# Optimization experiments

Measured on AMD Instinct MI355X. Metric: run time of the kernel, lower is better.

The kernel has to match this reference:

```python
import jax, jax.numpy as jnp
import numpy as np

B, S, D, H = 4, 2048, 1024, 4
HD = D // H


def setup_inputs() -> dict:
    key = jax.random.key(0)
    ks = jax.random.split(key, 6)
    s = 0.02  # init scale for projection weights
    return {
        "hidden_states": jax.random.normal(ks[0], (B, S, D), jnp.float32),
        "Wq": jax.random.normal(ks[1], (D, D), jnp.float32) * s,
        "Wk": jax.random.normal(ks[2], (D, D), jnp.float32) * s,
        "Wv": jax.random.normal(ks[3], (D, D), jnp.float32) * s,
        "Wo": jax.random.normal(ks[4], (D, D), jnp.float32) * s,
        "bo": jnp.zeros((D,), jnp.float32),
        "betas": jax.random.normal(ks[5], (1, H, 1, 1), jnp.float32),
        "mem": jnp.zeros((H, HD, HD), jnp.float32),
        "z": jnp.zeros((H, HD, 1), jnp.float32),
    }


def reference(hidden_states, Wq, Wk, Wv, Wo, bo, betas, mem, z):
    b, s, d = hidden_states.shape
    h = betas.shape[1]
    hd = d // h

    def split(x):  # [b,s,d] -> [b,h,s,hd]
        return x.reshape(b, s, h, hd).transpose(0, 2, 1, 3)

    q = split(hidden_states @ Wq.T)
    k = split(hidden_states @ Wk.T)
    v = split(hidden_states @ Wv.T)

    # standard causal attention (note: no 1/sqrt(d) scaling, faithful to source)
    aw = jnp.einsum('bhqd,bhkd->bhqk', q, k)
    causal = jnp.tril(jnp.ones((s, s), bool))
    aw = jnp.where(causal, aw, jnp.finfo(aw.dtype).min)
    p = jax.nn.softmax(aw, axis=-1)
    attn = jnp.einsum('bhqk,bhkd->bhqd', p, v)

    # linear-attention memory read
    sq = jax.nn.elu(q) + 1.0
    sk = jax.nn.elu(k) + 1.0
    A_mem = jnp.einsum('bhsd,hde->bhse', sq, mem) / (
        jnp.einsum('bhsd,hdo->bhso', sq, z) + 1e-6)

    # sigmoid-gated blend
    g = jax.nn.sigmoid(betas)
    out = g * A_mem + (1.0 - g) * attn

    # memory / z state update (delta rule), averaged over batch
    delta = jnp.einsum('bhsd,hde->bhse', sk, mem) / (
        jnp.einsum('bhsd,hdo->bhso', sk, z) + 1e-6)
    mem_new = mem + jnp.einsum('bhsd,bhse->hde', sk, v - delta) / b
    z_new = z + jnp.mean(jnp.sum(sk, axis=2), axis=0)[:, :, None]

    # merge heads + output projection
    out = out.transpose(0, 2, 1, 3).reshape(b, s, d)
    out = out @ Wo.T + bo
    return (out, mem_new, z_new)
```

## Files before the change

kernel.cpp:

```cpp
#include <hip/hip_runtime.h>

#define Bsz 4
#define Ssz 2048
#define Dsz 1024
#define Hsz 4
#define HDsz 256
#define Msz 8192

typedef unsigned short u16;
typedef __attribute__((ext_vector_type(8))) short bf16x8;
typedef __attribute__((ext_vector_type(4))) float f32x4;

__device__ __forceinline__ u16 f2b(float f) {
  unsigned u = __float_as_uint(f);
  return (u16)((u + 0x7FFFu + ((u >> 16) & 1u)) >> 16);
}
__device__ __forceinline__ unsigned pk2(float a, float b) {
  return (unsigned)f2b(a) | ((unsigned)f2b(b) << 16);
}

typedef const unsigned int __attribute__((address_space(1)))* gcp;
typedef unsigned int __attribute__((address_space(3)))* lcp;
__device__ __forceinline__ void gld16(const u16* g, u16* l) {
  __builtin_amdgcn_global_load_lds((gcp)g, (lcp)l, 16, 0, 0);
}

__global__ __launch_bounds__(256) void cvt_bf16(const float4* __restrict__ in,
                                                u16* __restrict__ outp) {
  size_t i = (size_t)blockIdx.x * 256 + threadIdx.x;
  float4 v = in[i];
  uint2 r; r.x = pk2(v.x, v.y); r.y = pk2(v.z, v.w);
  *(uint2*)(outp + i * 4) = r;
}

__global__ __launch_bounds__(256) void gemm_lds(const u16* __restrict__ A16,
                                                const u16* __restrict__ Wb,
                                                const float* __restrict__ bias,
                                                float* __restrict__ C32,
                                                u16* __restrict__ Cbf) {
  __shared__ u16 sA[128 * 32];
  __shared__ u16 sB[128 * 32];
  const int tid = threadIdx.x;
  const int lane = tid & 63, quad = lane >> 4, l15 = lane & 15;
  const int w = tid >> 6;
  const int mw = (w >> 1) * 64, nw = (w & 1) * 64;
  const int bid = blockIdx.y * 8 + blockIdx.x;
  const int nb = (bid & 7) * 64 + (bid >> 3);
  const int m0 = (nb >> 3) * 128, n0 = (nb & 7) * 128;
  const int r0 = tid >> 2, seg = (tid & 3) * 8;
  const u16* ga0 = A16 + (size_t)(m0 + r0) * Dsz + seg;
  const u16* gb0 = Wb + (size_t)(n0 + r0) * Dsz + seg;
  u16* lA0 = sA + w * 512;
  u16* lA1 = sA + 2048 + w * 512;
  u16* lB0 = sB + w * 512;
  u16* lB1 = sB + 2048 + w * 512;
  f32x4 acc[4][4] = {};
  for (int k0 = 0; k0 < Dsz; k0 += 32) {
    __syncthreads();
    gld16(ga0 + k0, lA0);
    gld16(ga0 + (size_t)64 * Dsz + k0, lA1);
    gld16(gb0 + k0, lB0);
    gld16(gb0 + (size_t)64 * Dsz + k0, lB1);
    __syncthreads();
    bf16x8 af[4], bfr[4];
#pragma unroll
    for (int i = 0; i < 4; ++i) {
      af[i] = *(const bf16x8*)&sA[(mw + i * 16 + l15) * 32 + quad * 8];
      bfr[i] = *(const bf16x8*)&sB[(nw + i * 16 + l15) * 32 + quad * 8];
    }
#pragma unroll
    for (int i = 0; i < 4; ++i)
#pragma unroll
      for (int j = 0; j < 4; ++j)
        acc[i][j] = __builtin_amdgcn_mfma_f32_16x16x32_bf16(af[i], bfr[j], acc[i][j], 0, 0, 0);
  }
#pragma unroll
  for (int j = 0; j < 4; ++j) {
    const int n = n0 + nw + j * 16 + l15;
    const float bv = bias ? bias[n] : 0.f;
#pragma unroll
    for (int i = 0; i < 4; ++i) {
#pragma unroll
      for (int r = 0; r < 4; ++r) {
        const int m = m0 + mw + i * 16 + quad * 4 + r;
        const float val = acc[i][j][r] + bv;
        const size_t idx = (size_t)m * Dsz + n;
        if (C32) C32[idx] = val;
        if (Cbf) Cbf[idx] = f2b(val);
      }
    }
  }
}

__global__ __launch_bounds__(256) void transpose_v(const float* __restrict__ V,
                                                   u16* __restrict__ Vt) {
  __shared__ u16 tile[32 * 36];
  const int t = threadIdx.x;
  const int s0 = blockIdx.x * 32, e0 = blockIdx.y * 32, bh = blockIdx.z;
  const int b = bh >> 2, h = bh & 3;
  {
    const int s_l = t >> 3, e8 = (t & 7) * 4;
    float4 v = *(const float4*)(V + ((size_t)(b * Ssz) + s0 + s_l) * Dsz + h * HDsz + e0 + e8);
    uint2 r; r.x = pk2(v.x, v.y); r.y = pk2(v.z, v.w);
    *(uint2*)&tile[s_l * 36 + e8] = r;
  }
  __syncthreads();
  {
    const int e_l = t >> 3, s4 = (t & 7) * 4;
    u16 a = tile[(s4 + 0) * 36 + e_l], b2 = tile[(s4 + 1) * 36 + e_l];
    u16 c = tile[(s4 + 2) * 36 + e_l], d = tile[(s4 + 3) * 36 + e_l];
    uint2 r; r.x = (unsigned)a | ((unsigned)b2 << 16);
    r.y = (unsigned)c | ((unsigned)d << 16);
    *(uint2*)(Vt + ((size_t)bh * HDsz + e0 + e_l) * Ssz + s0 + s4) = r;
  }
}

__global__ __launch_bounds__(256) void attn_mfma(const u16* __restrict__ Qg,
                                                 const u16* __restrict__ Kg,
                                                 const u16* __restrict__ Vtg,
                                                 float* __restrict__ At,
                                                 float* __restrict__ Pb,
                                                 float* __restrict__ mlb) {
  static const unsigned char tab[52] = {
      (unsigned char)(31|0x80), (unsigned char)(31|0xC0),
      (unsigned char)(30|0x80), (unsigned char)(30|0xC0),
      (unsigned char)(29|0x80), (unsigned char)(29|0xC0),
      (unsigned char)(28|0x80), (unsigned char)(28|0xC0),
      (unsigned char)(27|0x80), (unsigned char)(27|0xC0),
      (unsigned char)(26|0x80), (unsigned char)(26|0xC0),
      (unsigned char)(25|0x80), (unsigned char)(25|0xC0),
      (unsigned char)(24|0x80), (unsigned char)(24|0xC0),
      (unsigned char)(23|0x80), (unsigned char)(23|0xC0),
      11,
      (unsigned char)(22|0x80), (unsigned char)(22|0xC0),
      (unsigned char)(21|0x80), (unsigned char)(21|0xC0),
      10,
      (unsigned char)(20|0x80), (unsigned char)(20|0xC0),
      (unsigned char)(19|0x80), (unsigned char)(19|0xC0),
      9,
      (unsigned char)(18|0x80), (unsigned char)(18|0xC0),
      (unsigned char)(17|0x80), (unsigned char)(17|0xC0),
      8,
      (unsigned char)(16|0x80), (unsigned char)(16|0xC0),
      (unsigned char)(15|0x80), (unsigned char)(15|0xC0),
      7,
      (unsigned char)(14|0x80), (unsigned char)(14|0xC0),
      (unsigned char)(13|0x80), (unsigned char)(13|0xC0),
      6,
      (unsigned char)(12|0x80), (unsigned char)(12|0xC0),
      5, 4, 3, 2, 1, 0};
  const int e = tab[blockIdx.x];
  const int qt = e & 63, cc = (e >> 6) & 1;
  const bool split = (e >> 7) != 0;
  const int bh = blockIdx.y, b = bh >> 2, h = bh & 3;
  const int tid = threadIdx.x, w = tid >> 6, lane = tid & 63;
  const int quad = lane >> 4, l15 = lane & 15;
  __shared__ u16 sK[2][32 * 256];
  __shared__ u16 sV[256 * 32];
  const int q0w = qt * 64 + w * 16;
  bf16x8 qf[8];
  {
    const u16* qp = Qg + ((size_t)(b * Ssz) + q0w + l15) * Dsz + h * HDsz + quad * 8;
#pragma unroll
    for (int dd = 0; dd < 8; ++dd) qf[dd] = *(const bf16x8*)(qp + dd * 32);
  }
  f32x4 o[16] = {};
  float m_old = -1e30f, l = 0.f;
  const int nkt = 2 * qt + 2, half = qt + 1;
  const int kt_lo = (split && cc) ? half : 0;
  const int kt_hi = (split && !cc) ? half : nkt;
  const u16* kstage = Kg + ((size_t)(b * Ssz) + (tid >> 5)) * Dsz + h * HDsz
                      + (((tid & 31) ^ ((tid >> 5) & 7)) << 3);
  const u16* vstage = Vtg + ((size_t)bh * HDsz + (tid >> 2)) * Ssz
                      + (((tid & 3) ^ ((tid >> 3) & 3)) << 3);
  int bufc = 0;
  {
    const u16* kp = kstage + (size_t)(kt_lo * 32) * Dsz;
#pragma unroll
    for (int i = 0; i < 4; ++i)
      gld16(kp + (size_t)i * 8 * Dsz, &sK[0][w * 512 + i * 2048]);
  }
  for (int kt = kt_lo; kt < kt_hi; ++kt) {
    const int j0 = kt * 32;
    __syncthreads();
    {
      const u16* vp = vstage + kt * 32;
#pragma unroll
      for (int i = 0; i < 4; ++i)
        gld16(vp + (size_t)i * 64 * Ssz, &sV[w * 512 + i * 2048]);
    }
    if (kt + 1 < kt_hi) {
      const u16* kp = kstage + (size_t)((kt + 1) * 32) * Dsz;
      const int bn = bufc ^ 1;
#pragma unroll
      for (int i = 0; i < 4; ++i)
        gld16(kp + (size_t)i * 8 * Dsz, &sK[bn][w * 512 + i * 2048]);
    }
    f32x4 s0a = {}, s0b = {}, s1a = {}, s1b = {};
#pragma unroll
    for (int dd = 0; dd < 4; ++dd) {
      const int c0 = ((dd * 4 + quad) ^ (l15 & 7)) << 3;
      const int c1 = (((dd + 4) * 4 + quad) ^ (l15 & 7)) << 3;
      bf16x8 a0 = *(const bf16x8*)&sK[bufc][l15 * 256 + c0];
      bf16x8 a1 = *(const bf16x8*)&sK[bufc][(16 + l15) * 256 + c0];
      bf16x8 b0 = *(const bf16x8*)&sK[bufc][l15 * 256 + c1];
      bf16x8 b1 = *(const bf16x8*)&sK[bufc][(16 + l15) * 256 + c1];
      s0a = __builtin_amdgcn_mfma_f32_16x16x32_bf16(a0, qf[dd], s0a, 0, 0, 0);
      s1a = __builtin_amdgcn_mfma_f32_16x16x32_bf16(a1, qf[dd], s1a, 0, 0, 0);
      s0b = __builtin_amdgcn_mfma_f32_16x16x32_bf16(b0, qf[dd + 4], s0b, 0, 0, 0);
      s1b = __builtin_amdgcn_mfma_f32_16x16x32_bf16(b1, qf[dd + 4], s1b, 0, 0, 0);
    }
    f32x4 s0v = s0a + s0b, s1v = s1a + s1b;
    const int qg = q0w + l15;
    float p[8];
#pragma unroll
    for (int r = 0; r < 4; ++r) {
      const int kg = j0 + quad * 4 + r;
      p[r] = (kg <= qg) ? s0v[r] : -1e30f;
      p[4 + r] = (kg + 16 <= qg) ? s1v[r] : -1e30f;
    }
    float mt = p[0];
#pragma unroll
    for (int i = 1; i < 8; ++i) mt = fmaxf(mt, p[i]);
    mt = fmaxf(mt, __shfl_xor(mt, 16));
    mt = fmaxf(mt, __shfl_xor(mt, 32));
    const float m_new = fmaxf(m_old, mt);
    const float alpha = __expf(m_old - m_new);
    float ts = 0.f;
#pragma unroll
    for (int i = 0; i < 8; ++i) { p[i] = __expf(p[i] - m_new); ts += p[i]; }
    ts += __shfl_xor(ts, 16);
    ts += __shfl_xor(ts, 32);
    l = l * alpha + ts;
    m_old = m_new;
    if (!__all(alpha == 1.0f)) {
      const float a0_ = __shfl(alpha, (lane & 48) | (quad * 4 + 0));
      const float a1_ = __shfl(alpha, (lane & 48) | (quad * 4 + 1));
      const float a2_ = __shfl(alpha, (lane & 48) | (quad * 4 + 2));
      const float a3_ = __shfl(alpha, (lane & 48) | (quad * 4 + 3));
#pragma unroll
      for (int ds = 0; ds < 16; ++ds) {
        o[ds][0] *= a0_; o[ds][1] *= a1_; o[ds][2] *= a2_; o[ds][3] *= a3_;
      }
    }
    float xx[8];
#pragma unroll
    for (int i = 0; i < 8; ++i) xx[i] = __shfl_xor(p[i], 16);
    const bool qe = (quad & 1) == 0;
    float Alo[8], Ahi[8];
#pragma unroll
    for (int i = 0; i < 4; ++i) {
      Alo[i] = qe ? p[i] : xx[i];
      Alo[4 + i] = qe ? xx[i] : p[i];
      Ahi[i] = qe ? p[4 + i] : xx[4 + i];
      Ahi[4 + i] = qe ? xx[4 + i] : p[4 + i];
    }
    float zz[8];
    const bool sendlo = (quad & 1) != 0;
#pragma unroll
    for (int i = 0; i < 8; ++i) zz[i] = __shfl_xor(sendlo ? Alo[i] : Ahi[i], 32);
    float fin[8];
#pragma unroll
    for (int i = 0; i < 8; ++i)
      fin[i] = (quad == 0) ? Alo[i] : (quad == 3) ? Ahi[i] : zz[i];
    uint4 pkv;
    pkv.x = pk2(fin[0], fin[1]); pkv.y = pk2(fin[2], fin[3]);
    pkv.z = pk2(fin[4], fin[5]); pkv.w = pk2(fin[6], fin[7]);
    bf16x8 pf = *(bf16x8*)&pkv;
    const int vc0 = (quad ^ ((l15 >> 1) & 3)) << 3;
    __syncthreads();
#pragma unroll
    for (int ds = 0; ds < 16; ++ds) {
      bf16x8 bv = *(const bf16x8*)&sV[(ds * 16 + l15) * 32 + vc0];
      o[ds] = __builtin_amdgcn_mfma_f32_16x16x32_bf16(pf, bv, o[ds], 0, 0, 0);
    }
    bufc ^= 1;
  }
  if (!split) {
    float lr[4];
#pragma unroll
    for (int r = 0; r < 4; ++r) lr[r] = 1.f / __shfl(l, (lane & 48) | (quad * 4 + r));
    float* ob = At + ((size_t)bh * Ssz + q0w + quad * 4) * HDsz + l15;
#pragma unroll
    for (int r = 0; r < 4; ++r)
#pragma unroll
      for (int ds = 0; ds < 16; ++ds)
        ob[(size_t)r * HDsz + ds * 16] = o[ds][r] * lr[r];
  } else {
    float* dst;
    if (cc == 0)
      dst = At + ((size_t)bh * Ssz + q0w + quad * 4) * HDsz + l15;
    else
      dst = Pb + ((size_t)((bh * 20 + (qt - 12)) * 64) + w * 16 + quad * 4) * HDsz + l15;
#pragma unroll
    for (int r = 0; r < 4; ++r)
#pragma unroll
      for (int ds = 0; ds < 16; ++ds)
        dst[(size_t)r * HDsz + ds * 16] = o[ds][r];
    if (lane < 16) {
      const int idx = (bh * 20 + (qt - 12)) * 64 + w * 16 + l15;
      mlb[cc * 40960 + idx] = m_old;
      mlb[cc * 40960 + 20480 + idx] = l;
    }
  }
}

__global__ __launch_bounds__(256) void attn_merge(float* __restrict__ At,
                                                  const float* __restrict__ Pb,
                                                  const float* __restrict__ mlb) {
  const int qx = blockIdx.x, bh = blockIdx.y;
  const int t = threadIdx.x;
  const int slot = (bh * 20 + qx) * 64;
  float4* abase = (float4*)(At + ((size_t)bh * Ssz + (12 + qx) * 64) * HDsz);
  const float4* pbase = (const float4*)(Pb + (size_t)slot * HDsz);
#pragma unroll
  for (int i = 0; i < 16; ++i) {
    const int f = i * 256 + t;
    const int qr = f >> 6;
    const int idx = slot + qr;
    const float m0 = mlb[idx], l0 = mlb[20480 + idx];
    const float m1 = mlb[40960 + idx], l1 = mlb[61440 + idx];
    const float mm = fmaxf(m0, m1);
    const float w0 = __expf(m0 - mm), w1 = __expf(m1 - mm);
    const float inv = 1.f / (l0 * w0 + l1 * w1);
    float4 av = abase[f];
    float4 pv = pbase[f];
    float4 ov;
    ov.x = (av.x * w0 + pv.x * w1) * inv;
    ov.y = (av.y * w0 + pv.y * w1) * inv;
    ov.z = (av.z * w0 + pv.z * w1) * inv;
    ov.w = (av.w * w0 + pv.w * w1) * inv;
    abase[f] = ov;
  }
}

__global__ __launch_bounds__(256) void eludens(float* __restrict__ Qb,
                                               float* __restrict__ Kb,
                                               const float* __restrict__ z,
                                               float* __restrict__ dq,
                                               float* __restrict__ dk) {
  const int wid = threadIdx.x >> 6, lane = threadIdx.x & 63;
  const int r = blockIdx.x * 4 + wid;
  const int b = r >> 13, h = (r >> 11) & 3, s = r & 2047;
  const size_t base = ((size_t)(b * Ssz + s)) * Dsz + h * HDsz + lane * 4;
  float4 z4 = *(const float4*)(z + h * HDsz + lane * 4);
  float4 q = *(float4*)(Qb + base);
  q.x = q.x > 0.f ? q.x + 1.f : __expf(q.x);
  q.y = q.y > 0.f ? q.y + 1.f : __expf(q.y);
  q.z = q.z > 0.f ? q.z + 1.f : __expf(q.z);
  q.w = q.w > 0.f ? q.w + 1.f : __expf(q.w);
  *(float4*)(Qb + base) = q;
  float4 k = *(float4*)(Kb + base);
  k.x = k.x > 0.f ? k.x + 1.f : __expf(k.x);
  k.y = k.y > 0.f ? k.y + 1.f : __expf(k.y);
  k.z = k.z > 0.f ? k.z + 1.f : __expf(k.z);
  k.w = k.w > 0.f ? k.w + 1.f : __expf(k.w);
  *(float4*)(Kb + base) = k;
  float pq = q.x * z4.x + q.y * z4.y + q.z * z4.z + q.w * z4.w;
  float pk = k.x * z4.x + k.y * z4.y + k.z * z4.z + k.w * z4.w;
#pragma unroll
  for (int off = 32; off; off >>= 1) {
    pq += __shfl_down(pq, off);
    pk += __shfl_down(pk, off);
  }
  if (lane == 0) { dq[r] = pq; dk[r] = pk; }
}

__global__ __launch_bounds__(256) void memread_mfma(const float* __restrict__ Asrc,
                                                    const float* __restrict__ mem,
                                                    const float* __restrict__ dens,
                                                    const float* __restrict__ betas,
                                                    const float* __restrict__ At,
                                                    float* __restrict__ Vio,
                                                    u16* __restrict__ bfout, int mode) {
  const int h = blockIdx.z;
  const int tid = threadIdx.x, lane = tid & 63, w = tid >> 6;
  const int quad = lane >> 4, l15 = lane & 15;
  const int mw = (w >> 1) * 64, ew = (w & 1) * 64;
  const int m0 = blockIdx.y * 128, e0t = blockIdx.x * 128;
  __shared__ u16 sA[128 * 40];
  __shared__ u16 sB[128 * 40];
  const int srow = tid >> 1, sseg = (tid & 1) * 16;
  const int k4 = (tid & 7) * 4, e4 = (tid >> 3) * 4;
  f32x4 acc[4][4] = {};
  for (int k0 = 0; k0 < HDsz; k0 += 32) {
    __syncthreads();
    {
      const float* ap = Asrc + (size_t)(m0 + srow) * Dsz + h * HDsz + k0 + sseg;
      float4 f0 = *(const float4*)ap, f1 = *(const float4*)(ap + 4);
      float4 f2 = *(const float4*)(ap + 8), f3 = *(const float4*)(ap + 12);
      uint4 u0, u1;
      u0.x = pk2(f0.x, f0.y); u0.y = pk2(f0.z, f0.w);
      u0.z = pk2(f1.x, f1.y); u0.w = pk2(f1.z, f1.w);
      u1.x = pk2(f2.x, f2.y); u1.y = pk2(f2.z, f2.w);
      u1.z = pk2(f3.x, f3.y); u1.w = pk2(f3.z, f3.w);
      u16* dst = &sA[srow * 40 + sseg];
      *(uint4*)dst = u0; *(uint4*)(dst + 8) = u1;
    }
    {
      const float* bp = mem + (size_t)h * 65536 + (size_t)(k0 + k4) * HDsz + e0t + e4;
      float4 r0 = *(const float4*)bp;
      float4 r1 = *(const float4*)(bp + HDsz);
      float4 r2 = *(const float4*)(bp + 2 * HDsz);
      float4 r3 = *(const float4*)(bp + 3 * HDsz);
      const float* rr[4] = {(const float*)&r0, (const float*)&r1,
                            (const float*)&r2, (const float*)&r3};
#pragma unroll
      for (int c = 0; c < 4; ++c) {
        uint2 u;
        u.x = pk2(rr[0][c], rr[1][c]);
        u.y = pk2(rr[2][c], rr[3][c]);
        *(uint2*)&sB[(e4 + c) * 40 + k4] = u;
      }
    }
    __syncthreads();
    bf16x8 af[4], bfr[4];
#pragma unroll
    for (int i = 0; i < 4; ++i) {
      af[i] = *(const bf16x8*)&sA[(mw + i * 16 + l15) * 40 + quad * 8];
      bfr[i] = *(const bf16x8*)&sB[(ew + i * 16 + l15) * 40 + quad * 8];
    }
#pragma unroll
    for (int i = 0; i < 4; ++i)
#pragma unroll
      for (int j = 0; j < 4; ++j)
        acc[i][j] = __builtin_amdgcn_mfma_f32_16x16x32_bf16(af[i], bfr[j], acc[i][j], 0, 0, 0);
  }
  const float g = 1.f / (1.f + __expf(-betas[h]));
#pragma unroll
  for (int i = 0; i < 4; ++i) {
#pragma unroll
    for (int r = 0; r < 4; ++r) {
      const int m = m0 + mw + i * 16 + quad * 4 + r;
      const int b = m >> 11, s = m & 2047;
      const int rowidx = ((b << 2) + h) * Ssz + s;
      const float inv = 1.f / (dens[rowidx] + 1e-6f);
#pragma unroll
      for (int j = 0; j < 4; ++j) {
        const int e = e0t + ew + j * 16 + l15;
        const float av = acc[i][j][r] * inv;
        if (mode == 0) {
          const float a = At[(size_t)rowidx * HDsz + e];
          bfout[(size_t)m * Dsz + h * HDsz + e] = f2b(g * av + (1.f - g) * a);
        } else {
          float* p = Vio + (size_t)m * Dsz + h * HDsz + e;
          *p = *p - av;
        }
      }
    }
  }
}

__global__ __launch_bounds__(256) void mem_update_mfma(const float* __restrict__ SK,
                                                       const float* __restrict__ W,
                                                       float* __restrict__ P) {
  const int de = blockIdx.x;
  const int d0 = (de >> 1) * 128, e0 = (de & 1) * 128;
  const int h = blockIdx.y, chunk = blockIdx.z;
  const int m0 = chunk * 512;
  const int tid = threadIdx.x, lane = tid & 63, w = tid >> 6;
  const int quad = lane >> 4, l15 = lane & 15;
  const int dw = (w >> 1) * 64, ew = (w & 1) * 64;
  __shared__ u16 sA[128 * 40];
  __shared__ u16 sB[128 * 40];
  const int m4 = (tid & 7) * 4;
  const int c4 = (tid >> 3) * 4;
  f32x4 acc[4][4] = {};
  for (int mt = 0; mt < 512; mt += 32) {
    __syncthreads();
    const float* ka = SK + (size_t)(m0 + mt + m4) * Dsz + h * HDsz + d0 + c4;
    const float* wa = W + (size_t)(m0 + mt + m4) * Dsz + h * HDsz + e0 + c4;
    float4 a0 = *(const float4*)ka;
    float4 a1 = *(const float4*)(ka + Dsz);
    float4 a2 = *(const float4*)(ka + 2 * Dsz);
    float4 a3 = *(const float4*)(ka + 3 * Dsz);
    float4 b0 = *(const float4*)wa;
    float4 b1 = *(const float4*)(wa + Dsz);
    float4 b2 = *(const float4*)(wa + 2 * Dsz);
    float4 b3 = *(const float4*)(wa + 3 * Dsz);
    const float* aa[4] = {(const float*)&a0, (const float*)&a1,
                          (const float*)&a2, (const float*)&a3};
    const float* bb[4] = {(const float*)&b0, (const float*)&b1,
                          (const float*)&b2, (const float*)&b3};
#pragma unroll
    for (int c = 0; c < 4; ++c) {
      uint2 ua, ub2;
      ua.x = pk2(aa[0][c], aa[1][c]); ua.y = pk2(aa[2][c], aa[3][c]);
      ub2.x = pk2(bb[0][c], bb[1][c]); ub2.y = pk2(bb[2][c], bb[3][c]);
      *(uint2*)&sA[(c4 + c) * 40 + m4] = ua;
      *(uint2*)&sB[(c4 + c) * 40 + m4] = ub2;
    }
    __syncthreads();
    bf16x8 af[4], bfr[4];
#pragma unroll
    for (int i = 0; i < 4; ++i) {
      af[i] = *(const bf16x8*)&sA[(dw + i * 16 + l15) * 40 + quad * 8];
      bfr[i] = *(const bf16x8*)&sB[(ew + i * 16 + l15) * 40 + quad * 8];
    }
#pragma unroll
    for (int i = 0; i < 4; ++i)
#pragma unroll
      for (int j = 0; j < 4; ++j)
        acc[i][j] = __builtin_amdgcn_mfma_f32_16x16x32_bf16(af[i], bfr[j], acc[i][j], 0, 0, 0);
  }
  float* Pp = P + ((size_t)(h * 16 + chunk)) * 65536;
#pragma unroll
  for (int i = 0; i < 4; ++i)
#pragma unroll
    for (int r = 0; r < 4; ++r) {
      const int d = d0 + dw + i * 16 + quad * 4 + r;
#pragma unroll
      for (int j = 0; j < 4; ++j) {
        const int e = e0 + ew + j * 16 + l15;
        Pp[(size_t)d * HDsz + e] = acc[i][j][r];
      }
    }
}

__global__ __launch_bounds__(256) void mem_reduce(const float4* __restrict__ P,
                                                  const float4* __restrict__ mem,
                                                  float4* __restrict__ outmem) {
  const int gid = blockIdx.x * 256 + threadIdx.x;
  const int h = gid >> 14, off = gid & 16383;
  float sx = 0.f, sy = 0.f, sz = 0.f, sw = 0.f;
#pragma unroll 4
  for (int c = 0; c < 16; ++c) {
    float4 v = P[((size_t)(h * 16 + c) << 14) + off];
    sx += v.x; sy += v.y; sz += v.z; sw += v.w;
  }
  float4 m = mem[gid];
  float4 o;
  o.x = m.x + 0.25f * sx; o.y = m.y + 0.25f * sy;
  o.z = m.z + 0.25f * sz; o.w = m.w + 0.25f * sw;
  outmem[gid] = o;
}

__global__ __launch_bounds__(256) void z_update(const float* __restrict__ SK,
                                                const float* __restrict__ z_in,
                                                float* __restrict__ z_out) {
  __shared__ float4 red[256];
  const int h = blockIdx.x >> 7, chunk = blockIdx.x & 127;
  const int wid = threadIdx.x >> 6, lane = threadIdx.x & 63;
  const int m0 = chunk * 64;
  float4 s = {0.f, 0.f, 0.f, 0.f};
#pragma unroll
  for (int i = 0; i < 16; ++i) {
    const int row = m0 + i * 4 + wid;
    float4 v = *(const float4*)(SK + (size_t)row * Dsz + h * HDsz + lane * 4);
    s.x += v.x; s.y += v.y; s.z += v.z; s.w += v.w;
  }
  red[wid * 64 + lane] = s;
  __syncthreads();
  if (wid == 0) {
    float4 a = red[lane], b = red[64 + lane], c = red[128 + lane], d = red[192 + lane];
    a.x = (a.x + b.x + c.x + d.x) * 0.25f;
    a.y = (a.y + b.y + c.y + d.y) * 0.25f;
    a.z = (a.z + b.z + c.z + d.z) * 0.25f;
    a.w = (a.w + b.w + c.w + d.w) * 0.25f;
    if (chunk == 0) {
      const float4 z4 = *(const float4*)(z_in + h * HDsz + lane * 4);
      a.x += z4.x; a.y += z4.y; a.z += z4.z; a.w += z4.w;
    }
    float* zp = z_out + h * HDsz + lane * 4;
    atomicAdd(zp + 0, a.x);
    atomicAdd(zp + 1, a.y);
    atomicAdd(zp + 2, a.z);
    atomicAdd(zp + 3, a.w);
  }
}

extern "C" void kernel_launch(void* const* d_in, const int* in_sizes, int n_in,
                              void* d_out, int out_size, void* d_ws, size_t ws_size,
                              hipStream_t stream) {
  (void)in_sizes; (void)n_in; (void)out_size; (void)ws_size;
  const float* Hs = (const float*)d_in[0];
  const float* Wq = (const float*)d_in[1];
  const float* Wk = (const float*)d_in[2];
  const float* Wv = (const float*)d_in[3];
  const float* Wo = (const float*)d_in[4];
  const float* bo = (const float*)d_in[5];
  const float* betas = (const float*)d_in[6];
  const float* mem = (const float*)d_in[7];
  const float* z = (const float*)d_in[8];

  float* ws = (float*)d_ws;
  float* Qb = ws;
  float* Kb = ws + 8388608;
  float* Vb = ws + 16777216;
  float* At = ws + 25165824;
  float* dq = ws + 33554432;
  float* dk = ws + 33587200;
  float* mlb = ws + 33619968;
  u16* ub = (u16*)(ws + 33701888);
  u16* Wqb = ub;
  u16* Wkb = ub + 1048576;
  u16* Wvb = ub + 2097152;
  u16* Wob = ub + 3145728;
  u16* Qbf = ub + 4194304;
  u16* Kbf = ub + 12582912;
  u16* Vt = ub + 20971520;
  u16* Hsb = Vt;
  float* P = (float*)Vt;
  float* Pb = (float*)d_out;

  float* out = (float*)d_out;
  float* outmem = out + (size_t)Msz * Dsz;
  float* outz = outmem + Hsz * HDsz * HDsz;

  hipMemsetAsync(outz, 0, (size_t)(Hsz * HDsz) * sizeof(float), stream);

  cvt_bf16<<<1024, 256, 0, stream>>>((const float4*)Wq, Wqb);
  cvt_bf16<<<1024, 256, 0, stream>>>((const float4*)Wk, Wkb);
  cvt_bf16<<<1024, 256, 0, stream>>>((const float4*)Wv, Wvb);
  cvt_bf16<<<1024, 256, 0, stream>>>((const float4*)Wo, Wob);
  cvt_bf16<<<8192, 256, 0, stream>>>((const float4*)Hs, Hsb);

  dim3 gg(8, 64);
  gemm_lds<<<gg, 256, 0, stream>>>(Hsb, Wqb, nullptr, Qb, Qbf);
  gemm_lds<<<gg, 256, 0, stream>>>(Hsb, Wkb, nullptr, Kb, Kbf);
  gemm_lds<<<gg, 256, 0, stream>>>(Hsb, Wvb, nullptr, Vb, nullptr);

  transpose_v<<<dim3(64, 8, 16), 256, 0, stream>>>(Vb, Vt);
  attn_mfma<<<dim3(52, 16), 256, 0, stream>>>(Qbf, Kbf, Vt, At, Pb, mlb);
  attn_merge<<<dim3(20, 16), 256, 0, stream>>>(At, Pb, mlb);

  eludens<<<8192, 256, 0, stream>>>(Qb, Kb, z, dq, dk);

  memread_mfma<<<dim3(2, 64, 4), 256, 0, stream>>>(Qb, mem, dq, betas, At, nullptr, Qbf, 0);
  memread_mfma<<<dim3(2, 64, 4), 256, 0, stream>>>(Kb, mem, dk, betas, nullptr, Vb, nullptr, 1);

  mem_update_mfma<<<dim3(4, 4, 16), 256, 0, stream>>>(Kb, Vb, P);
  mem_reduce<<<256, 256, 0, stream>>>((const float4*)P, (const float4*)mem, (float4*)outmem);
  z_update<<<512, 256, 0, stream>>>(Kb, z, outz);

  gemm_lds<<<gg, 256, 0, stream>>>(Qbf, Wob, bo, out, nullptr);
}
```

Before: 523.7 us.

## Deepen GEMM K-tile with swizzled LDS and streamline attention softmax

The GEMM now stages a 64-wide K slice per iteration with an XOR-swizzled LDS layout. This halves the number of barrier pairs and aims to avoid bank conflicts on fragment reads. The attention softmax switches to base-2 exponentials by folding log2(e) into the bf16 Q copy. It also skips rescaling of the running max unless the max grows by more than a threshold, and packs P to bf16 before a cheaper shuffle-based layout exchange. The lazy-rescale threshold risks larger intermediate values, and the merge kernel now uses exp2 on maxima that live in the log2 domain.

```diff
diff --git a/kernel.cpp b/kernel.cpp
--- a/kernel.cpp
+++ b/kernel.cpp
@@ -6,6 +6,7 @@
 #define Hsz 4
 #define HDsz 256
 #define Msz 8192
+#define LOG2E 1.4426950408889634f
 
 typedef unsigned short u16;
 typedef __attribute__((ext_vector_type(8))) short bf16x8;
@@ -17,6 +18,13 @@
 }
 __device__ __forceinline__ unsigned pk2(float a, float b) {
   return (unsigned)f2b(a) | ((unsigned)f2b(b) << 16);
+}
+__device__ __forceinline__ float ex2(float x) {
+#if __has_builtin(__builtin_amdgcn_exp2f)
+  return __builtin_amdgcn_exp2f(x);
+#else
+  return exp2f(x);
+#endif
 }
 
 typedef const unsigned int __attribute__((address_space(1)))* gcp;
@@ -37,9 +45,10 @@
                                                 const u16* __restrict__ Wb,
                                                 const float* __restrict__ bias,
                                                 float* __restrict__ C32,
-                                                u16* __restrict__ Cbf) {
-  __shared__ u16 sA[128 * 32];
-  __shared__ u16 sB[128 * 32];
+                                                u16* __restrict__ Cbf,
+                                                float cbfs) {
+  __shared__ u16 sA[128 * 64];
+  __shared__ u16 sB[128 * 64];
   const int tid = threadIdx.x;
   const int lane = tid & 63, quad = lane >> 4, l15 = lane & 15;
   const int w = tid >> 6;
@@ -47,32 +56,34 @@
   const int bid = blockIdx.y * 8 + blockIdx.x;
   const int nb = (bid & 7) * 64 + (bid >> 3);
   const int m0 = (nb >> 3) * 128, n0 = (nb & 7) * 128;
-  const int r0 = tid >> 2, seg = (tid & 3) * 8;
+  const int r0 = tid >> 3;
+  const int seg = ((tid & 7) ^ (r0 & 7)) * 8;
   const u16* ga0 = A16 + (size_t)(m0 + r0) * Dsz + seg;
   const u16* gb0 = Wb + (size_t)(n0 + r0) * Dsz + seg;
-  u16* lA0 = sA + w * 512;
-  u16* lA1 = sA + 2048 + w * 512;
-  u16* lB0 = sB + w * 512;
-  u16* lB1 = sB + 2048 + w * 512;
   f32x4 acc[4][4] = {};
-  for (int k0 = 0; k0 < Dsz; k0 += 32) {
-    __syncthreads();
-    gld16(ga0 + k0, lA0);
-    gld16(ga0 + (size_t)64 * Dsz + k0, lA1);
-    gld16(gb0 + k0, lB0);
-    gld16(gb0 + (size_t)64 * Dsz + k0, lB1);
-    __syncthreads();
-    bf16x8 af[4], bfr[4];
+  for (int k0 = 0; k0 < Dsz; k0 += 64) {
+    __syncthreads();
 #pragma unroll
     for (int i = 0; i < 4; ++i) {
-      af[i] = *(const bf16x8*)&sA[(mw + i * 16 + l15) * 32 + quad * 8];
-      bfr[i] = *(const bf16x8*)&sB[(nw + i * 16 + l15) * 32 + quad * 8];
-    }
-#pragma unroll
-    for (int i = 0; i < 4; ++i)
-#pragma unroll
-      for (int j = 0; j < 4; ++j)
-        acc[i][j] = __builtin_amdgcn_mfma_f32_16x16x32_bf16(af[i], bfr[j], acc[i][j], 0, 0, 0);
+      gld16(ga0 + (size_t)(i * 32) * Dsz + k0, sA + i * 2048 + w * 512);
+      gld16(gb0 + (size_t)(i * 32) * Dsz + k0, sB + i * 2048 + w * 512);
+    }
+    __syncthreads();
+#pragma unroll
+    for (int dd = 0; dd < 2; ++dd) {
+      bf16x8 af[4], bfr[4];
+#pragma unroll
+      for (int i = 0; i < 4; ++i) {
+        const int sl = ((quad + 4 * dd) ^ (l15 & 7)) * 8;
+        af[i] = *(const bf16x8*)&sA[(mw + i * 16 + l15) * 64 + sl];
+        bfr[i] = *(const bf16x8*)&sB[(nw + i * 16 + l15) * 64 + sl];
+      }
+#pragma unroll
+      for (int i = 0; i < 4; ++i)
+#pragma unroll
+        for (int j = 0; j < 4; ++j)
+          acc[i][j] = __builtin_amdgcn_mfma_f32_16x16x32_bf16(af[i], bfr[j], acc[i][j], 0, 0, 0);
+    }
   }
 #pragma unroll
   for (int j = 0; j < 4; ++j) {
@@ -86,7 +97,7 @@
         const float val = acc[i][j][r] + bv;
         const size_t idx = (size_t)m * Dsz + n;
         if (C32) C32[idx] = val;
-        if (Cbf) Cbf[idx] = f2b(val);
+        if (Cbf) Cbf[idx] = f2b(val * cbfs);
       }
     }
   }
@@ -219,21 +230,23 @@
       p[r] = (kg <= qg) ? s0v[r] : -1e30f;
       p[4 + r] = (kg + 16 <= qg) ? s1v[r] : -1e30f;
     }
-    float mt = p[0];
-#pragma unroll
-    for (int i = 1; i < 8; ++i) mt = fmaxf(mt, p[i]);
+    float mt = fmaxf(fmaxf(fmaxf(p[0], p[1]), fmaxf(p[2], p[3])),
+                     fmaxf(fmaxf(p[4], p[5]), fmaxf(p[6], p[7])));
     mt = fmaxf(mt, __shfl_xor(mt, 16));
     mt = fmaxf(mt, __shfl_xor(mt, 32));
-    const float m_new = fmaxf(m_old, mt);
-    const float alpha = __expf(m_old - m_new);
+    const bool keep = __all(mt - m_old <= 11.0f);
+    const float m_new = keep ? m_old : fmaxf(m_old, mt);
     float ts = 0.f;
 #pragma unroll
-    for (int i = 0; i < 8; ++i) { p[i] = __expf(p[i] - m_new); ts += p[i]; }
+    for (int i = 0; i < 8; ++i) { p[i] = ex2(p[i] - m_new); ts += p[i]; }
     ts += __shfl_xor(ts, 16);
     ts += __shfl_xor(ts, 32);
-    l = l * alpha + ts;
-    m_old = m_new;
-    if (!__all(alpha == 1.0f)) {
+    if (keep) {
+      l += ts;
+    } else {
+      const float alpha = ex2(m_old - m_new);
+      l = l * alpha + ts;
+      m_old = m_new;
       const float a0_ = __shfl(alpha, (lane & 48) | (quad * 4 + 0));
       const float a1_ = __shfl(alpha, (lane & 48) | (quad * 4 + 1));
       const float a2_ = __shfl(alpha, (lane & 48) | (quad * 4 + 2));
@@ -243,29 +256,20 @@
         o[ds][0] *= a0_; o[ds][1] *= a1_; o[ds][2] *= a2_; o[ds][3] *= a3_;
       }
     }
-    float xx[8];
-#pragma unroll
-    for (int i = 0; i < 8; ++i) xx[i] = __shfl_xor(p[i], 16);
-    const bool qe = (quad & 1) == 0;
-    float Alo[8], Ahi[8];
-#pragma unroll
-    for (int i = 0; i < 4; ++i) {
-      Alo[i] = qe ? p[i] : xx[i];
-      Alo[4 + i] = qe ? xx[i] : p[i];
-      Ahi[i] = qe ? p[4 + i] : xx[4 + i];
-      Ahi[4 + i] = qe ? xx[4 + i] : p[4 + i];
-    }
-    float zz[8];
-    const bool sendlo = (quad & 1) != 0;
-#pragma unroll
-    for (int i = 0; i < 8; ++i) zz[i] = __shfl_xor(sendlo ? Alo[i] : Ahi[i], 32);
-    float fin[8];
-#pragma unroll
-    for (int i = 0; i < 8; ++i)
-      fin[i] = (quad == 0) ? Alo[i] : (quad == 3) ? Ahi[i] : zz[i];
+    const unsigned a0p = pk2(p[0], p[1]), a1p = pk2(p[2], p[3]);
+    const unsigned b0p = pk2(p[4], p[5]), b1p = pk2(p[6], p[7]);
+    const int sAl = l15 | ((quad & 1) << 5);
+    const int sBl = sAl | 16;
+    const unsigned xa0 = __shfl(a0p, sAl), xa1 = __shfl(a1p, sAl);
+    const unsigned xb0 = __shfl(b0p, sAl), xb1 = __shfl(b1p, sAl);
+    const unsigned ya0 = __shfl(a0p, sBl), ya1 = __shfl(a1p, sBl);
+    const unsigned yb0 = __shfl(b0p, sBl), yb1 = __shfl(b1p, sBl);
+    const bool hi2 = quad >= 2;
     uint4 pkv;
-    pkv.x = pk2(fin[0], fin[1]); pkv.y = pk2(fin[2], fin[3]);
-    pkv.z = pk2(fin[4], fin[5]); pkv.w = pk2(fin[6], fin[7]);
+    pkv.x = hi2 ? xb0 : xa0;
+    pkv.y = hi2 ? xb1 : xa1;
+    pkv.z = hi2 ? yb0 : ya0;
+    pkv.w = hi2 ? yb1 : ya1;
     bf16x8 pf = *(bf16x8*)&pkv;
     const int vc0 = (quad ^ ((l15 >> 1) & 3)) << 3;
     __syncthreads();
@@ -321,7 +325,7 @@
     const float m0 = mlb[idx], l0 = mlb[20480 + idx];
     const float m1 = mlb[40960 + idx], l1 = mlb[61440 + idx];
     const float mm = fmaxf(m0, m1);
-    const float w0 = __expf(m0 - mm), w1 = __expf(m1 - mm);
+    const float w0 = ex2(m0 - mm), w1 = ex2(m1 - mm);
     const float inv = 1.f / (l0 * w0 + l1 * w1);
     float4 av = abase[f];
     float4 pv = pbase[f];
@@ -616,9 +620,9 @@
   cvt_bf16<<<8192, 256, 0, stream>>>((const float4*)Hs, Hsb);
 
   dim3 gg(8, 64);
-  gemm_lds<<<gg, 256, 0, stream>>>(Hsb, Wqb, nullptr, Qb, Qbf);
-  gemm_lds<<<gg, 256, 0, stream>>>(Hsb, Wkb, nullptr, Kb, Kbf);
-  gemm_lds<<<gg, 256, 0, stream>>>(Hsb, Wvb, nullptr, Vb, nullptr);
+  gemm_lds<<<gg, 256, 0, stream>>>(Hsb, Wqb, nullptr, Qb, Qbf, LOG2E);
+  gemm_lds<<<gg, 256, 0, stream>>>(Hsb, Wkb, nullptr, Kb, Kbf, 1.f);
+  gemm_lds<<<gg, 256, 0, stream>>>(Hsb, Wvb, nullptr, Vb, nullptr, 1.f);
 
   transpose_v<<<dim3(64, 8, 16), 256, 0, stream>>>(Vb, Vt);
   attn_mfma<<<dim3(52, 16), 256, 0, stream>>>(Qbf, Kbf, Vt, At, Pb, mlb);
@@ -633,5 +637,5 @@
   mem_reduce<<<256, 256, 0, stream>>>((const float4*)P, (const float4*)mem, (float4*)outmem);
   z_update<<<512, 256, 0, stream>>>(Kb, z, outz);
 
-  gemm_lds<<<gg, 256, 0, stream>>>(Qbf, Wob, bo, out, nullptr);
-}
+  gemm_lds<<<gg, 256, 0, stream>>>(Qbf, Wob, bo, out, nullptr, 1.f);
+}
```

Measured after the change: 498.8 us. 4.8% less time.
